# Performance work log

Measured on AMD Instinct MI355X. Metric: run time of the kernel, lower is better.

The kernel has to match this reference:

```python
import jax, jax.numpy as jnp
import numpy as np

B, IN, OUT = 512, 4096, 11008


def setup_inputs() -> dict:
    key = jax.random.key(0)
    k_x, k_stored, k_sign, k_scale, k_bias = jax.random.split(key, 5)
    x = jax.random.normal(k_x, (B, IN), dtype=jnp.float32)
    # QINS encoding: stored uint8 magnitude in [1, 255], sign in {-1, +1}
    stored = jax.random.randint(k_stored, (OUT, IN), 1, 256, dtype=jnp.int32)
    sign = 2 * jax.random.randint(k_sign, (OUT, IN), 0, 2, dtype=jnp.int32) - 1
    # log-range from from_linear's fallback calibration: weights in [e^-10, e^0]
    log_min = jnp.asarray(-10.0, dtype=jnp.float32)
    log_max = jnp.asarray(0.0, dtype=jnp.float32)
    # per-channel calibration scale, clamped to [0.5, 2.0] in from_linear
    scale = jax.random.uniform(k_scale, (OUT,), dtype=jnp.float32, minval=0.5, maxval=2.0)
    bias = jax.random.normal(k_bias, (OUT,), dtype=jnp.float32) * 0.01
    return {"x": x, "stored": stored, "sign": sign, "log_min": log_min,
            "log_max": log_max, "scale": scale, "bias": bias}


def reference(x, stored, sign, log_min, log_max, scale, bias):
    # Reconstruct fp32 weight from log-scale uint8 encoding (QINS)
    normalized = (255.0 - stored.astype(jnp.float32)) / 254.0      # [OUT, IN]
    log_w = log_min + normalized * (log_max - log_min)
    weight = sign.astype(jnp.float32) * jnp.exp(log_w)             # [OUT, IN]
    # y = (x @ W^T + b) * scale   (per-output-channel scale)
    out = jnp.einsum('bi,oi->bo', x, weight) + bias
    return out * scale
```

## Files before the change

kernel.cpp:

```cpp
#include <hip/hip_runtime.h>
#include <hip/hip_bf16.h>

#define B_DIM   512
#define IN_DIM  4096
#define OUT_DIM 11008

typedef __bf16 bf16x4 __attribute__((ext_vector_type(4)));
typedef __bf16 bf16x8 __attribute__((ext_vector_type(8)));
typedef float  floatx4 __attribute__((ext_vector_type(4)));

__global__ __launch_bounds__(256) void decode_w_kernel(
    const int* __restrict__ stored, const int* __restrict__ sign,
    const float* __restrict__ logmin, const float* __restrict__ logmax,
    __bf16* __restrict__ w) {
  int idx = blockIdx.x * blockDim.x + threadIdx.x;
  float lmin  = logmin[0];
  float slope = (logmax[0] - lmin) * (1.0f / 254.0f);
  int4 s = ((const int4*)stored)[idx];
  int4 g = ((const int4*)sign)[idx];
  float w0 = __expf(lmin + (float)(255 - s.x) * slope) * (float)g.x;
  float w1 = __expf(lmin + (float)(255 - s.y) * slope) * (float)g.y;
  float w2 = __expf(lmin + (float)(255 - s.z) * slope) * (float)g.z;
  float w3 = __expf(lmin + (float)(255 - s.w) * slope) * (float)g.w;
  bf16x4 o;
  o[0] = (__bf16)w0; o[1] = (__bf16)w1; o[2] = (__bf16)w2; o[3] = (__bf16)w3;
  ((bf16x4*)w)[idx] = o;
}

__global__ __launch_bounds__(256) void conv_x_kernel(
    const float* __restrict__ x, __bf16* __restrict__ xb) {
  int idx = blockIdx.x * blockDim.x + threadIdx.x;
  float4 v = ((const float4*)x)[idx];
  bf16x4 o;
  o[0] = (__bf16)v.x; o[1] = (__bf16)v.y; o[2] = (__bf16)v.z; o[3] = (__bf16)v.w;
  ((bf16x4*)xb)[idx] = o;
}

__device__ __forceinline__ void gl_lds16(const __bf16* g, __bf16* l) {
  __builtin_amdgcn_global_load_lds(
      (const __attribute__((address_space(1))) void*)g,
      (__attribute__((address_space(3))) void*)l, 16, 0, 0);
}

__global__ __launch_bounds__(256, 2) void gemm_bt_kernel(
    const __bf16* __restrict__ A,
    const __bf16* __restrict__ Bw,
    const float* __restrict__ scale, const float* __restrict__ bias,
    float* __restrict__ out) {
  constexpr int K = IN_DIM, N = OUT_DIM;
  constexpr int BM = 128, BN = 128, BK = 32;

  __shared__ __align__(16) __bf16 sA[BM * BK];
  __shared__ __align__(16) __bf16 sB[BN * BK];

  const int tid  = threadIdx.x;
  const int lane = tid & 63;
  const int wave = tid >> 6;
  const int wm   = (wave >> 1) * 64;
  const int wn   = (wave & 1) * 64;
  const int m16  = lane & 15;
  const int q    = lane >> 4;

  const int bn0 = blockIdx.x * BN;
  const int bm0 = blockIdx.y * BM;

  const int r0 = tid >> 2;
  const int c0 = (tid & 3) * 8;
  const __bf16* gA0 = A  + (bm0 + r0) * K + c0;
  const __bf16* gA1 = A  + (bm0 + r0 + 64) * K + c0;
  const __bf16* gB0 = Bw + (bn0 + r0) * K + c0;
  const __bf16* gB1 = Bw + (bn0 + r0 + 64) * K + c0;
  __bf16* lA0 = sA + tid * 8;
  __bf16* lA1 = sA + 2048 + tid * 8;
  __bf16* lB0 = sB + tid * 8;
  __bf16* lB1 = sB + 2048 + tid * 8;

  floatx4 acc[4][4] = {};

  for (int kt = 0; kt < K; kt += BK) {
    __syncthreads();
    gl_lds16(gA0 + kt, lA0);
    gl_lds16(gA1 + kt, lA1);
    gl_lds16(gB0 + kt, lB0);
    gl_lds16(gB1 + kt, lB1);
    __syncthreads();

    bf16x8 afr[4], bfr[4];
#pragma unroll
    for (int i = 0; i < 4; ++i)
      afr[i] = *(const bf16x8*)&sA[(wm + i * 16 + m16) * BK + q * 8];
#pragma unroll
    for (int i = 0; i < 4; ++i)
      bfr[i] = *(const bf16x8*)&sB[(wn + i * 16 + m16) * BK + q * 8];

#pragma unroll
    for (int mi = 0; mi < 4; ++mi)
#pragma unroll
      for (int ni = 0; ni < 4; ++ni)
        acc[mi][ni] = __builtin_amdgcn_mfma_f32_16x16x32_bf16(
            afr[mi], bfr[ni], acc[mi][ni], 0, 0, 0);
  }

#pragma unroll
  for (int ni = 0; ni < 4; ++ni) {
    const int col = bn0 + wn + ni * 16 + m16;
    const float sc = scale[col];
    const float bb = bias[col] * sc;
#pragma unroll
    for (int mi = 0; mi < 4; ++mi) {
#pragma unroll
      for (int r = 0; r < 4; ++r) {
        const int row = bm0 + wm + mi * 16 + q * 4 + r;
        out[row * N + col] = acc[mi][ni][r] * sc + bb;
      }
    }
  }
}

extern "C" void kernel_launch(void* const* d_in, const int* in_sizes, int n_in,
                              void* d_out, int out_size, void* d_ws, size_t ws_size,
                              hipStream_t stream) {
  const float* x      = (const float*)d_in[0];
  const int*   stored = (const int*)d_in[1];
  const int*   sign   = (const int*)d_in[2];
  const float* logmin = (const float*)d_in[3];
  const float* logmax = (const float*)d_in[4];
  const float* scale  = (const float*)d_in[5];
  const float* bias   = (const float*)d_in[6];
  float* out = (float*)d_out;

  __bf16* wsW = (__bf16*)d_ws;
  __bf16* wsX = wsW + (size_t)OUT_DIM * IN_DIM;

  decode_w_kernel<<<(OUT_DIM * (IN_DIM / 4)) / 256, 256, 0, stream>>>(
      stored, sign, logmin, logmax, wsW);
  conv_x_kernel<<<(B_DIM * (IN_DIM / 4)) / 256, 256, 0, stream>>>(x, wsX);
  gemm_bt_kernel<<<dim3(OUT_DIM / 128, B_DIM / 128), 256, 0, stream>>>(
      wsX, wsW, scale, bias, out);
}
```

Before: 468.1 us.

## Fuse weight decoding into GEMM with full-batch tiles per output block

Removes the separate weight-decode kernel and its bf16 weight buffer, and decodes stored/sign int32 values into LDS inside the GEMM main loop. Each block now covers all 512 batch rows for 64 output columns with 512 threads, so every weight element is decoded exactly once and the int32 weights are read once. This avoids writing and re-reading an intermediate bf16 weight matrix. The cost is exp and conversion work sitting on the GEMM critical path with no prefetch overlap, a larger 32KB A tile per block, and only 172 blocks for 256 CUs.

```diff
diff --git a/kernel.cpp b/kernel.cpp
--- a/kernel.cpp
+++ b/kernel.cpp
@@ -8,24 +8,6 @@
 typedef __bf16 bf16x4 __attribute__((ext_vector_type(4)));
 typedef __bf16 bf16x8 __attribute__((ext_vector_type(8)));
 typedef float  floatx4 __attribute__((ext_vector_type(4)));
-
-__global__ __launch_bounds__(256) void decode_w_kernel(
-    const int* __restrict__ stored, const int* __restrict__ sign,
-    const float* __restrict__ logmin, const float* __restrict__ logmax,
-    __bf16* __restrict__ w) {
-  int idx = blockIdx.x * blockDim.x + threadIdx.x;
-  float lmin  = logmin[0];
-  float slope = (logmax[0] - lmin) * (1.0f / 254.0f);
-  int4 s = ((const int4*)stored)[idx];
-  int4 g = ((const int4*)sign)[idx];
-  float w0 = __expf(lmin + (float)(255 - s.x) * slope) * (float)g.x;
-  float w1 = __expf(lmin + (float)(255 - s.y) * slope) * (float)g.y;
-  float w2 = __expf(lmin + (float)(255 - s.z) * slope) * (float)g.z;
-  float w3 = __expf(lmin + (float)(255 - s.w) * slope) * (float)g.w;
-  bf16x4 o;
-  o[0] = (__bf16)w0; o[1] = (__bf16)w1; o[2] = (__bf16)w2; o[3] = (__bf16)w3;
-  ((bf16x4*)w)[idx] = o;
-}
 
 __global__ __launch_bounds__(256) void conv_x_kernel(
     const float* __restrict__ x, __bf16* __restrict__ xb) {
@@ -42,56 +24,70 @@
       (__attribute__((address_space(3))) void*)l, 16, 0, 0);
 }
 
-__global__ __launch_bounds__(256, 2) void gemm_bt_kernel(
+__global__ __launch_bounds__(512, 2) void fused_gemm_kernel(
     const __bf16* __restrict__ A,
-    const __bf16* __restrict__ Bw,
+    const int* __restrict__ stored,
+    const int* __restrict__ sign,
+    const float* __restrict__ logmin, const float* __restrict__ logmax,
     const float* __restrict__ scale, const float* __restrict__ bias,
     float* __restrict__ out) {
   constexpr int K = IN_DIM, N = OUT_DIM;
-  constexpr int BM = 128, BN = 128, BK = 32;
+  constexpr int BK = 32;
 
-  __shared__ __align__(16) __bf16 sA[BM * BK];
-  __shared__ __align__(16) __bf16 sB[BN * BK];
+  __shared__ __align__(16) __bf16 sA[512 * BK];
+  __shared__ __align__(16) __bf16 sB[64 * BK];
 
   const int tid  = threadIdx.x;
   const int lane = tid & 63;
   const int wave = tid >> 6;
-  const int wm   = (wave >> 1) * 64;
-  const int wn   = (wave & 1) * 64;
   const int m16  = lane & 15;
   const int q    = lane >> 4;
 
-  const int bn0 = blockIdx.x * BN;
-  const int bm0 = blockIdx.y * BM;
+  const int bn0 = blockIdx.x * 64;
 
-  const int r0 = tid >> 2;
-  const int c0 = (tid & 3) * 8;
-  const __bf16* gA0 = A  + (bm0 + r0) * K + c0;
-  const __bf16* gA1 = A  + (bm0 + r0 + 64) * K + c0;
-  const __bf16* gB0 = Bw + (bn0 + r0) * K + c0;
-  const __bf16* gB1 = Bw + (bn0 + r0 + 64) * K + c0;
-  __bf16* lA0 = sA + tid * 8;
-  __bf16* lA1 = sA + 2048 + tid * 8;
-  __bf16* lB0 = sB + tid * 8;
-  __bf16* lB1 = sB + 2048 + tid * 8;
+  const float lmin  = logmin[0];
+  const float slope = (logmax[0] - lmin) * (1.0f / 254.0f);
+
+  const int ar = tid >> 2;
+  const int ac = (tid & 3) * 8;
+  const __bf16* gA = A + (size_t)ar * K + ac;
+  __bf16* lA = sA + tid * 8;
+
+  const int br = tid >> 3;
+  const int bc = (tid & 7) * 4;
+  const int* gS = stored + (size_t)(bn0 + br) * K + bc;
+  const int* gG = sign   + (size_t)(bn0 + br) * K + bc;
+  __bf16* lB = sB + tid * 4;
 
   floatx4 acc[4][4] = {};
 
   for (int kt = 0; kt < K; kt += BK) {
+    int4 s = *(const int4*)(gS + kt);
+    int4 g = *(const int4*)(gG + kt);
+
     __syncthreads();
-    gl_lds16(gA0 + kt, lA0);
-    gl_lds16(gA1 + kt, lA1);
-    gl_lds16(gB0 + kt, lB0);
-    gl_lds16(gB1 + kt, lB1);
+
+    gl_lds16(gA + kt,             lA);
+    gl_lds16(gA + kt + 128 * K,   lA + 4096);
+    gl_lds16(gA + kt + 256 * K,   lA + 8192);
+    gl_lds16(gA + kt + 384 * K,   lA + 12288);
+
+    bf16x4 wv;
+    wv[0] = (__bf16)(__expf(lmin + (float)(255 - s.x) * slope) * (float)g.x);
+    wv[1] = (__bf16)(__expf(lmin + (float)(255 - s.y) * slope) * (float)g.y);
+    wv[2] = (__bf16)(__expf(lmin + (float)(255 - s.z) * slope) * (float)g.z);
+    wv[3] = (__bf16)(__expf(lmin + (float)(255 - s.w) * slope) * (float)g.w);
+    *(bf16x4*)lB = wv;
+
     __syncthreads();
 
     bf16x8 afr[4], bfr[4];
 #pragma unroll
     for (int i = 0; i < 4; ++i)
-      afr[i] = *(const bf16x8*)&sA[(wm + i * 16 + m16) * BK + q * 8];
+      afr[i] = *(const bf16x8*)&sA[(wave * 64 + i * 16 + m16) * BK + q * 8];
 #pragma unroll
     for (int i = 0; i < 4; ++i)
-      bfr[i] = *(const bf16x8*)&sB[(wn + i * 16 + m16) * BK + q * 8];
+      bfr[i] = *(const bf16x8*)&sB[(i * 16 + m16) * BK + q * 8];
 
 #pragma unroll
     for (int mi = 0; mi < 4; ++mi)
@@ -103,15 +99,15 @@
 
 #pragma unroll
   for (int ni = 0; ni < 4; ++ni) {
-    const int col = bn0 + wn + ni * 16 + m16;
+    const int col = bn0 + ni * 16 + m16;
     const float sc = scale[col];
     const float bb = bias[col] * sc;
 #pragma unroll
     for (int mi = 0; mi < 4; ++mi) {
 #pragma unroll
       for (int r = 0; r < 4; ++r) {
-        const int row = bm0 + wm + mi * 16 + q * 4 + r;
-        out[row * N + col] = acc[mi][ni][r] * sc + bb;
+        const int row = wave * 64 + mi * 16 + q * 4 + r;
+        out[(size_t)row * N + col] = acc[mi][ni][r] * sc + bb;
       }
     }
   }
@@ -129,12 +125,9 @@
   const float* bias   = (const float*)d_in[6];
   float* out = (float*)d_out;
 
-  __bf16* wsW = (__bf16*)d_ws;
-  __bf16* wsX = wsW + (size_t)OUT_DIM * IN_DIM;
+  __bf16* wsX = (__bf16*)d_ws;
 
-  decode_w_kernel<<<(OUT_DIM * (IN_DIM / 4)) / 256, 256, 0, stream>>>(
-      stored, sign, logmin, logmax, wsW);
   conv_x_kernel<<<(B_DIM * (IN_DIM / 4)) / 256, 256, 0, stream>>>(x, wsX);
-  gemm_bt_kernel<<<dim3(OUT_DIM / 128, B_DIM / 128), 256, 0, stream>>>(
-      wsX, wsW, scale, bias, out);
+  fused_gemm_kernel<<<OUT_DIM / 64, 512, 0, stream>>>(
+      wsX, stored, sign, logmin, logmax, scale, bias, out);
 }
```

Measured after the change: 476.7 us. About the same (+1.8%).
